# Kernel optimization log

Hardware: AMD Instinct MI355X
Metric: run time of the kernel (lower is better)

## Reference

```python
import jax, jax.numpy as jnp
import numpy as np


def setup_inputs() -> dict:
    key = jax.random.key(0)
    ks = jax.random.split(key, 6)
    B, Cin, H, W = 8, 512, 128, 128
    Ck, Cv, K = 256, 256, 64
    s = lambda fan: fan ** -0.5
    return {
        "x": jax.random.normal(ks[0], (B, Cin, H, W), jnp.float32),
        "context": jax.random.normal(ks[1], (B, Cv, K), jnp.float32),
        "Wq": jax.random.normal(ks[2], (Ck, Cin), jnp.float32) * s(Cin),
        "Wk": jax.random.normal(ks[3], (Ck, Cv), jnp.float32) * s(Cv),
        "Wv": jax.random.normal(ks[4], (Cv, Cv), jnp.float32) * s(Cv),
        "Wp": jax.random.normal(ks[5], (Cin, Cv), jnp.float32) * s(Cv),
    }


def reference(x, context, Wq, Wk, Wv, Wp):
    B, Cin, H, W = x.shape
    Ck = Wq.shape[0]
    scale = Ck ** -0.5
    xf = x.reshape(B, Cin, H * W)                      # [B, Cin, N]
    q = jnp.einsum("kc,bcn->bnk", Wq, xf)             # [B, N, Ck]
    k = jnp.einsum("kc,bcm->bkm", Wk, context)        # [B, Ck, K]
    v = jnp.einsum("vc,bcm->bmv", Wv, context)        # [B, K, Cv]
    sim = jnp.einsum("bnk,bkm->bnm", q, k) * scale    # [B, N, K]
    attn = jax.nn.softmax(sim, axis=-1)
    out = jnp.einsum("bnm,bmv->bnv", attn, v)         # [B, N, Cv]
    out = jnp.einsum("cv,bnv->bcn", Wp, out)          # [B, Cin, N]
    return out.reshape(B, Cin, H, W)
```

## Files before the change

### kernel.cpp

```cpp
#include <hip/hip_runtime.h>
#include <stdint.h>

#define B_    8
#define CIN   512
#define NPIX  16384
#define CK    256
#define KCTX  64
#define CV    256

typedef _Float16 f16;
typedef _Float16 f16x4 __attribute__((ext_vector_type(4)));
typedef _Float16 f16x8 __attribute__((ext_vector_type(8)));
typedef float    f32x4 __attribute__((ext_vector_type(4)));

#define LOG2E 1.44269504f

#define WQKT_OFF 0
#define WPV_OFF  524288
#define KF_OFF   1048576
#define VM_OFF   1310720

__device__ __forceinline__ void gl_lds16(const void* g, void* l) {
    __builtin_amdgcn_global_load_lds(
        (const __attribute__((address_space(1))) uint32_t*)g,
        (__attribute__((address_space(3))) uint32_t*)l, 16, 0, 0);
}

__global__ __launch_bounds__(1024) void prep1(const float* __restrict__ ctx,
                                              const float* __restrict__ Wk,
                                              const float* __restrict__ Wv,
                                              char* __restrict__ ws) {
    const int p = blockIdx.x;
    const int b = blockIdx.y;
    const int t = threadIdx.x;
    const int m = t & 63;
    const int rg = t >> 6;
    const int row = (p & 15) * 16 + rg;
    const bool is_k = (p < 16);
    const float* W = (is_k ? Wk : Wv) + (size_t)row * CV;
    const float* cb = ctx + (size_t)b * CV * KCTX + m;
    float acc = 0.f;
    #pragma unroll 8
    for (int c = 0; c < CV; ++c)
        acc = fmaf(W[c], cb[(size_t)c * KCTX], acc);
    char* dst = ws + (is_k ? KF_OFF : VM_OFF) + b * 32768 + (row * 64 + m) * 2;
    *(f16*)dst = (f16)acc;
}

__global__ __launch_bounds__(1024) void prep2(const float* __restrict__ Wq,
                                              const float* __restrict__ Wp,
                                              char* __restrict__ ws) {
    const int p = blockIdx.x;
    const int b = blockIdx.y;
    const int t = threadIdx.x;
    const int m = t & 63;
    const int cg = t >> 6;
    float acc[4] = {0.f, 0.f, 0.f, 0.f};
    if (p < 8) {
        const int cb = p * 64 + cg * 4;
        const f16* kf = (const f16*)(ws + KF_OFF + b * 32768) + m;
        for (int kk = 0; kk < CK; ++kk) {
            f32x4 wv = *(const f32x4*)(Wq + (size_t)kk * CIN + cb);
            float kv = (float)kf[kk * 64];
            #pragma unroll
            for (int i = 0; i < 4; ++i) acc[i] = fmaf(wv[i], kv, acc[i]);
        }
        char* base = ws + WQKT_OFF + b * 65536;
        #pragma unroll
        for (int i = 0; i < 4; ++i) {
            int c = cb + i;
            int byte = (c >> 6) * 8192 + m * 128 + 16 * (((c >> 3) & 7) ^ (m & 7)) + 2 * (c & 7);
            *(f16*)(base + byte) = (f16)(acc[i] * 0.0625f);
        }
    } else {
        const int cb = (p - 8) * 64 + cg * 4;
        const f16* vm = (const f16*)(ws + VM_OFF + b * 32768) + m;
        for (int v = 0; v < CV; v += 4) {
            f32x4 wp[4];
            #pragma unroll
            for (int i = 0; i < 4; ++i)
                wp[i] = *(const f32x4*)(Wp + (size_t)(cb + i) * CV + v);
            #pragma unroll
            for (int j = 0; j < 4; ++j) {
                float vv = (float)vm[(v + j) * 64];
                #pragma unroll
                for (int i = 0; i < 4; ++i) acc[i] = fmaf(wp[i][j], vv, acc[i]);
            }
        }
        char* base = ws + WPV_OFF + b * 65536;
        #pragma unroll
        for (int i = 0; i < 4; ++i) {
            int c = cb + i;
            int byte = (c >> 7) * 16384 + (c & 127) * 128 + 16 * (((m >> 3) & 7) ^ (c & 7)) + 2 * (m & 7);
            *(f16*)(base + byte) = (f16)acc[i];
        }
    }
}

__global__ __launch_bounds__(256, 2) void fused(const float* __restrict__ x,
                                                const char* __restrict__ ws,
                                                float* __restrict__ out) {
    __shared__ char lds[73728];
    char* x_s   = lds;
    char* wq_s  = lds + 16384;
    char* at_s  = lds + 32768;
    char* wpv_s = lds + 40960;

    const int b  = blockIdx.y;
    const int n0 = blockIdx.x * 64;
    const int t  = threadIdx.x;
    const int w  = t >> 6, l = t & 63, g = l >> 4, ln = l & 15;

    const float* xb = x + (size_t)b * CIN * NPIX + n0;
    const char* wqkt_g = ws + WQKT_OFF + b * 65536;
    const char* wpv_g  = ws + WPV_OFF  + b * 65536;

    const int n4 = (t & 15) * 4;
    const int c4 = (t >> 4) * 4;
    const int xsw = 16 * (((c4 >> 3) & 7)) + 2 * (c4 & 7);

    f32x4 xr[4];
    {
        const float* xp = xb + (size_t)c4 * NPIX + n4;
        #pragma unroll
        for (int i = 0; i < 4; ++i) xr[i] = *(const f32x4*)(xp + (size_t)i * NPIX);
    }
    #pragma unroll
    for (int r = 0; r < 2; ++r) {
        int ch = t + 256 * r;
        gl_lds16(wqkt_g + ch * 16, wq_s + ch * 16);
    }
    #pragma unroll
    for (int j = 0; j < 4; ++j) {
        f16x4 v4; v4[0] = (f16)xr[0][j]; v4[1] = (f16)xr[1][j]; v4[2] = (f16)xr[2][j]; v4[3] = (f16)xr[3][j];
        int n = n4 + j;
        *(f16x4*)(x_s + n * 128 + (xsw ^ (16 * (n & 7)))) = v4;
    }
    __syncthreads();

    f32x4 accs[4] = {};
    const int nB = 16 * w + ln;
    for (int s = 0; s < 8; ++s) {
        char* xc = x_s + (s & 1) * 8192;
        char* wc = wq_s + (s & 1) * 8192;
        if (s < 7) {
            char* wn = wq_s + ((s + 1) & 1) * 8192;
            #pragma unroll
            for (int r = 0; r < 2; ++r) {
                int ch = t + 256 * r;
                gl_lds16(wqkt_g + (s + 1) * 8192 + ch * 16, wn + ch * 16);
            }
            const float* xp = xb + (size_t)((s + 1) * 64 + c4) * NPIX + n4;
            #pragma unroll
            for (int i = 0; i < 4; ++i) xr[i] = *(const f32x4*)(xp + (size_t)i * NPIX);
        }
        #pragma unroll
        for (int kk = 0; kk < 2; ++kk) {
            int kb = kk * 4 + g;
            f16x8 bf = *(const f16x8*)(xc + nB * 128 + 16 * (kb ^ (nB & 7)));
            #pragma unroll
            for (int mi = 0; mi < 4; ++mi) {
                int mm = 16 * mi + ln;
                f16x8 af = *(const f16x8*)(wc + mm * 128 + 16 * (kb ^ (mm & 7)));
                accs[mi] = __builtin_amdgcn_mfma_f32_16x16x32_f16(af, bf, accs[mi], 0, 0, 0);
            }
        }
        if (s < 7) {
            char* xn = x_s + ((s + 1) & 1) * 8192;
            #pragma unroll
            for (int j = 0; j < 4; ++j) {
                f16x4 v4; v4[0] = (f16)xr[0][j]; v4[1] = (f16)xr[1][j]; v4[2] = (f16)xr[2][j]; v4[3] = (f16)xr[3][j];
                int n = n4 + j;
                *(f16x4*)(xn + n * 128 + (xsw ^ (16 * (n & 7)))) = v4;
            }
        }
        __syncthreads();
    }

    float mx = accs[0][0];
    #pragma unroll
    for (int mi = 0; mi < 4; ++mi)
        #pragma unroll
        for (int r = 0; r < 4; ++r) mx = fmaxf(mx, accs[mi][r]);
    mx = fmaxf(mx, __shfl_xor(mx, 16, 64));
    mx = fmaxf(mx, __shfl_xor(mx, 32, 64));
    float pv[4][4];
    float sum = 0.f;
    #pragma unroll
    for (int mi = 0; mi < 4; ++mi)
        #pragma unroll
        for (int r = 0; r < 4; ++r) {
            float pe = __builtin_amdgcn_exp2f((accs[mi][r] - mx) * LOG2E);
            pv[mi][r] = pe; sum += pe;
        }
    sum += __shfl_xor(sum, 16, 64);
    sum += __shfl_xor(sum, 32, 64);
    float inv = 1.f / sum;
    #pragma unroll
    for (int mi = 0; mi < 4; ++mi) {
        f16x4 a4;
        #pragma unroll
        for (int r = 0; r < 4; ++r) a4[r] = (f16)(pv[mi][r] * inv);
        int m4 = 16 * mi + 4 * g;
        *(f16x4*)(at_s + nB * 128 + 16 * (((m4 >> 3) & 7) ^ (nB & 7)) + 2 * (m4 & 7)) = a4;
    }
    #pragma unroll
    for (int r = 0; r < 4; ++r) {
        int ch = t + 256 * r;
        gl_lds16(wpv_g + ch * 16, wpv_s + ch * 16);
    }
    __syncthreads();

    float* ob = out + (size_t)b * CIN * NPIX + n0 + 16 * w + ln;
    #pragma unroll 1
    for (int s5 = 0; s5 < 4; ++s5) {
        char* pc = wpv_s + (s5 & 1) * 16384;
        if (s5 < 3) {
            char* pn = wpv_s + ((s5 + 1) & 1) * 16384;
            #pragma unroll
            for (int r = 0; r < 4; ++r) {
                int ch = t + 256 * r;
                gl_lds16(wpv_g + (s5 + 1) * 16384 + ch * 16, pn + ch * 16);
            }
        }
        f16x8 bf[2];
        #pragma unroll
        for (int kk = 0; kk < 2; ++kk)
            bf[kk] = *(const f16x8*)(at_s + nB * 128 + 16 * ((kk * 4 + g) ^ (nB & 7)));
        #pragma unroll
        for (int mi = 0; mi < 8; ++mi) {
            f32x4 acc = {};
            int cl = 16 * mi + ln;
            #pragma unroll
            for (int kk = 0; kk < 2; ++kk) {
                f16x8 af = *(const f16x8*)(pc + cl * 128 + 16 * ((kk * 4 + g) ^ (cl & 7)));
                acc = __builtin_amdgcn_mfma_f32_16x16x32_f16(af, bf[kk], acc, 0, 0, 0);
            }
            int cg0 = s5 * 128 + 16 * mi + 4 * g;
            #pragma unroll
            for (int r = 0; r < 4; ++r)
                ob[(size_t)(cg0 + r) * NPIX] = acc[r];
        }
        __syncthreads();
    }
}

extern "C" void kernel_launch(void* const* d_in, const int* in_sizes, int n_in,
                              void* d_out, int out_size, void* d_ws, size_t ws_size,
                              hipStream_t stream) {
    (void)in_sizes; (void)n_in; (void)out_size; (void)ws_size;
    const float* x   = (const float*)d_in[0];
    const float* ctx = (const float*)d_in[1];
    const float* Wq  = (const float*)d_in[2];
    const float* Wk  = (const float*)d_in[3];
    const float* Wv  = (const float*)d_in[4];
    const float* Wp  = (const float*)d_in[5];
    float* out = (float*)d_out;
    char* ws = (char*)d_ws;

    prep1<<<dim3(32, B_), 1024, 0, stream>>>(ctx, Wk, Wv, ws);
    prep2<<<dim3(16, B_), 1024, 0, stream>>>(Wq, Wp, ws);
    fused<<<dim3(NPIX / 64, B_), 256, 0, stream>>>(x, ws, out);
}
```

Before: 176.3 us.

## Double pixel tile to 128 with 512 threads and register-resident attention for projection

Each block now covers 128 pixels with 8 waves. The softmax output stays in registers as MFMA A-operands, so the separate attention LDS buffer is gone. The whole 64KB Wp·V slab is loaded into LDS once, reusing the x buffer, so the old 4-stage double-buffered output loop is dropped. The output is written as contiguous float4 nontemporal stores along pixels instead of strided scalar stores. The Wp·V layout in prep and the LDS swizzle are also changed to match. The aims are fewer syncs, better store coalescing and halved per-block weight loads, at the cost of more LDS per block and possibly lower occupancy.

```diff
diff --git a/kernel.cpp b/kernel.cpp
--- a/kernel.cpp
+++ b/kernel.cpp
@@ -88,76 +88,71 @@
             }
         }
         char* base = ws + WPV_OFF + b * 65536;
+        const int slot = (m >> 5) * 4 + ((m >> 2) & 3);
+        const int jj   = ((m >> 4) & 1) * 4 + (m & 3);
         #pragma unroll
         for (int i = 0; i < 4; ++i) {
             int c = cb + i;
-            int byte = (c >> 7) * 16384 + (c & 127) * 128 + 16 * (((m >> 3) & 7) ^ (c & 7)) + 2 * (m & 7);
-            *(f16*)(base + byte) = (f16)acc[i];
-        }
-    }
-}
-
-__global__ __launch_bounds__(256, 2) void fused(const float* __restrict__ x,
+            *(f16*)(base + c * 128 + 16 * (slot ^ (c & 7)) + 2 * jj) = (f16)acc[i];
+        }
+    }
+}
+
+__global__ __launch_bounds__(512, 4) void fused(const float* __restrict__ x,
                                                 const char* __restrict__ ws,
                                                 float* __restrict__ out) {
-    __shared__ char lds[73728];
-    char* x_s   = lds;
-    char* wq_s  = lds + 16384;
-    char* at_s  = lds + 32768;
-    char* wpv_s = lds + 40960;
+    __shared__ char lds[65536];
+    char* x_s  = lds;
+    char* wq_s = lds + 32768;
 
     const int b  = blockIdx.y;
-    const int n0 = blockIdx.x * 64;
+    const int n0 = blockIdx.x * 128;
     const int t  = threadIdx.x;
     const int w  = t >> 6, l = t & 63, g = l >> 4, ln = l & 15;
+    const int nB = 16 * w + ln;
+    const int fnB = (nB ^ (nB >> 3)) & 7;
 
     const float* xb = x + (size_t)b * CIN * NPIX + n0;
     const char* wqkt_g = ws + WQKT_OFF + b * 65536;
     const char* wpv_g  = ws + WPV_OFF  + b * 65536;
 
-    const int n4 = (t & 15) * 4;
-    const int c4 = (t >> 4) * 4;
-    const int xsw = 16 * (((c4 >> 3) & 7)) + 2 * (c4 & 7);
-
+    const int n4 = (t & 31) * 4;
+    const int c4 = (t >> 5) * 4;
+    const int cslot = (c4 >> 3) & 7;
+    const int coff  = 2 * (c4 & 7);
+
+    gl_lds16(wqkt_g + t * 16, wq_s + t * 16);
     f32x4 xr[4];
     {
         const float* xp = xb + (size_t)c4 * NPIX + n4;
         #pragma unroll
-        for (int i = 0; i < 4; ++i) xr[i] = *(const f32x4*)(xp + (size_t)i * NPIX);
-    }
-    #pragma unroll
-    for (int r = 0; r < 2; ++r) {
-        int ch = t + 256 * r;
-        gl_lds16(wqkt_g + ch * 16, wq_s + ch * 16);
+        for (int i = 0; i < 4; ++i)
+            xr[i] = __builtin_nontemporal_load((const f32x4*)(xp + (size_t)i * NPIX));
     }
     #pragma unroll
     for (int j = 0; j < 4; ++j) {
         f16x4 v4; v4[0] = (f16)xr[0][j]; v4[1] = (f16)xr[1][j]; v4[2] = (f16)xr[2][j]; v4[3] = (f16)xr[3][j];
         int n = n4 + j;
-        *(f16x4*)(x_s + n * 128 + (xsw ^ (16 * (n & 7)))) = v4;
+        int fn = (n ^ (n >> 3)) & 7;
+        *(f16x4*)(x_s + n * 128 + 16 * (cslot ^ fn) + coff) = v4;
     }
     __syncthreads();
 
     f32x4 accs[4] = {};
-    const int nB = 16 * w + ln;
     for (int s = 0; s < 8; ++s) {
-        char* xc = x_s + (s & 1) * 8192;
-        char* wc = wq_s + (s & 1) * 8192;
+        const char* xc = x_s + (s & 1) * 16384;
+        const char* wc = wq_s + (s & 1) * 8192;
         if (s < 7) {
-            char* wn = wq_s + ((s + 1) & 1) * 8192;
-            #pragma unroll
-            for (int r = 0; r < 2; ++r) {
-                int ch = t + 256 * r;
-                gl_lds16(wqkt_g + (s + 1) * 8192 + ch * 16, wn + ch * 16);
-            }
+            gl_lds16(wqkt_g + (s + 1) * 8192 + t * 16, wq_s + ((s + 1) & 1) * 8192 + t * 16);
             const float* xp = xb + (size_t)((s + 1) * 64 + c4) * NPIX + n4;
             #pragma unroll
-            for (int i = 0; i < 4; ++i) xr[i] = *(const f32x4*)(xp + (size_t)i * NPIX);
+            for (int i = 0; i < 4; ++i)
+                xr[i] = __builtin_nontemporal_load((const f32x4*)(xp + (size_t)i * NPIX));
         }
         #pragma unroll
         for (int kk = 0; kk < 2; ++kk) {
             int kb = kk * 4 + g;
-            f16x8 bf = *(const f16x8*)(xc + nB * 128 + 16 * (kb ^ (nB & 7)));
+            f16x8 bf = *(const f16x8*)(xc + nB * 128 + 16 * (kb ^ fnB));
             #pragma unroll
             for (int mi = 0; mi < 4; ++mi) {
                 int mm = 16 * mi + ln;
@@ -166,15 +161,22 @@
             }
         }
         if (s < 7) {
-            char* xn = x_s + ((s + 1) & 1) * 8192;
+            char* xn = x_s + ((s + 1) & 1) * 16384;
             #pragma unroll
             for (int j = 0; j < 4; ++j) {
                 f16x4 v4; v4[0] = (f16)xr[0][j]; v4[1] = (f16)xr[1][j]; v4[2] = (f16)xr[2][j]; v4[3] = (f16)xr[3][j];
                 int n = n4 + j;
-                *(f16x4*)(xn + n * 128 + (xsw ^ (16 * (n & 7)))) = v4;
+                int fn = (n ^ (n >> 3)) & 7;
+                *(f16x4*)(xn + n * 128 + 16 * (cslot ^ fn) + coff) = v4;
             }
         }
         __syncthreads();
+    }
+
+    #pragma unroll
+    for (int r = 0; r < 8; ++r) {
+        int ch = t + 512 * r;
+        gl_lds16(wpv_g + ch * 16, lds + ch * 16);
     }
 
     float mx = accs[0][0];
@@ -196,52 +198,26 @@
     sum += __shfl_xor(sum, 16, 64);
     sum += __shfl_xor(sum, 32, 64);
     float inv = 1.f / sum;
-    #pragma unroll
-    for (int mi = 0; mi < 4; ++mi) {
-        f16x4 a4;
-        #pragma unroll
-        for (int r = 0; r < 4; ++r) a4[r] = (f16)(pv[mi][r] * inv);
-        int m4 = 16 * mi + 4 * g;
-        *(f16x4*)(at_s + nB * 128 + 16 * (((m4 >> 3) & 7) ^ (nB & 7)) + 2 * (m4 & 7)) = a4;
-    }
-    #pragma unroll
-    for (int r = 0; r < 4; ++r) {
-        int ch = t + 256 * r;
-        gl_lds16(wpv_g + ch * 16, wpv_s + ch * 16);
-    }
+
+    f16x8 afr[2];
+    #pragma unroll
+    for (int kk = 0; kk < 2; ++kk)
+        #pragma unroll
+        for (int j = 0; j < 8; ++j)
+            afr[kk][j] = (f16)(pv[2 * kk + (j >> 2)][j & 3] * inv);
     __syncthreads();
 
-    float* ob = out + (size_t)b * CIN * NPIX + n0 + 16 * w + ln;
-    #pragma unroll 1
-    for (int s5 = 0; s5 < 4; ++s5) {
-        char* pc = wpv_s + (s5 & 1) * 16384;
-        if (s5 < 3) {
-            char* pn = wpv_s + ((s5 + 1) & 1) * 16384;
-            #pragma unroll
-            for (int r = 0; r < 4; ++r) {
-                int ch = t + 256 * r;
-                gl_lds16(wpv_g + (s5 + 1) * 16384 + ch * 16, pn + ch * 16);
-            }
-        }
-        f16x8 bf[2];
-        #pragma unroll
-        for (int kk = 0; kk < 2; ++kk)
-            bf[kk] = *(const f16x8*)(at_s + nB * 128 + 16 * ((kk * 4 + g) ^ (nB & 7)));
-        #pragma unroll
-        for (int mi = 0; mi < 8; ++mi) {
-            f32x4 acc = {};
-            int cl = 16 * mi + ln;
-            #pragma unroll
-            for (int kk = 0; kk < 2; ++kk) {
-                f16x8 af = *(const f16x8*)(pc + cl * 128 + 16 * ((kk * 4 + g) ^ (cl & 7)));
-                acc = __builtin_amdgcn_mfma_f32_16x16x32_f16(af, bf[kk], acc, 0, 0, 0);
-            }
-            int cg0 = s5 * 128 + 16 * mi + 4 * g;
-            #pragma unroll
-            for (int r = 0; r < 4; ++r)
-                ob[(size_t)(cg0 + r) * NPIX] = acc[r];
-        }
-        __syncthreads();
+    float* ob = out + (size_t)b * CIN * NPIX + n0 + 16 * w + 4 * g;
+    #pragma unroll 4
+    for (int ct = 0; ct < 32; ++ct) {
+        int c = 16 * ct + ln;
+        f32x4 acc = {};
+        #pragma unroll
+        for (int kk = 0; kk < 2; ++kk) {
+            f16x8 bf = *(const f16x8*)(lds + c * 128 + 16 * ((kk * 4 + g) ^ (c & 7)));
+            acc = __builtin_amdgcn_mfma_f32_16x16x32_f16(afr[kk], bf, acc, 0, 0, 0);
+        }
+        __builtin_nontemporal_store(acc, (f32x4*)(ob + (size_t)c * NPIX));
     }
 }
 
@@ -260,5 +236,5 @@
 
     prep1<<<dim3(32, B_), 1024, 0, stream>>>(ctx, Wk, Wv, ws);
     prep2<<<dim3(16, B_), 1024, 0, stream>>>(Wq, Wp, ws);
-    fused<<<dim3(NPIX / 64, B_), 256, 0, stream>>>(x, ws, out);
-}
+    fused<<<dim3(NPIX / 128, B_), 512, 0, stream>>>(x, ws, out);
+}
```

Result: slower. 188.3 us (+6.8%).
